# Optimization experiments

Hardware: AMD Instinct MI355X
Metric: run time of the kernel (lower is better)

Reference implementation:

```python
import jax, jax.numpy as jnp
import numpy as np

B, L, H, ED, NCONV = 64, 2048, 128, 4, 3
N = B * L


def gat(x, src, dst, edge_attr, W, a_s, a_d, We, a_e, b, self_loops):
    """PyG GATConv, heads=1, concat=True, negative_slope=0.2, fill_value='mean'."""
    n = x.shape[0]
    h = x @ W                              # [N,H]
    a_src = h @ a_s                        # [N]
    a_dst = h @ a_d                        # [N]
    alpha = a_src[src] + a_dst[dst] + (edge_attr @ We) @ a_e  # [E]
    if self_loops:
        ones = jnp.ones(src.shape[0], x.dtype)
        deg = jax.ops.segment_sum(ones, dst, num_segments=n)
        mean_attr = jax.ops.segment_sum(edge_attr, dst, num_segments=n) / jnp.maximum(deg, 1.0)[:, None]
        loop_alpha = a_src + a_dst + (mean_attr @ We) @ a_e
        idx = jnp.arange(n, dtype=src.dtype)
        src = jnp.concatenate([src, idx])
        dst = jnp.concatenate([dst, idx])
        alpha = jnp.concatenate([alpha, loop_alpha])
    alpha = jax.nn.leaky_relu(alpha, 0.2)
    m = jax.ops.segment_max(alpha, dst, num_segments=n)
    ex = jnp.exp(alpha - m[dst])
    den = jax.ops.segment_sum(ex, dst, num_segments=n)
    coef = ex / jnp.maximum(den, 1e-16)[dst]
    return jax.ops.segment_sum(coef[:, None] * h[src], dst, num_segments=n) + b


def setup_inputs() -> dict:
    key = jax.random.key(0)
    ks = iter(jax.random.split(key, 32))
    # binary trees: per graph, node k>0 has parent (k-1)//2; edge child->parent (to_up)
    local = np.arange(1, L)
    parent = (local - 1) // 2
    offs = (np.arange(B) * L)[:, None]
    src = jnp.asarray((local[None, :] + offs).ravel(), dtype=jnp.int32)
    dst = jnp.asarray((parent[None, :] + offs).ravel(), dtype=jnp.int32)
    E = src.shape[0]
    s = 0.1
    inp = {
        "x": jax.random.normal(next(ks), (N,), jnp.float32),
        "src": src,
        "dst": dst,
        "edge_attr": jax.random.normal(next(ks), (E, ED), jnp.float32),
        "up_W0": jax.random.normal(next(ks), (1, H)) * s,
        "up_W": jax.random.normal(next(ks), (NCONV - 1, H, H)) * s,
        "up_att_src": jax.random.normal(next(ks), (NCONV, H)) * s,
        "up_att_dst": jax.random.normal(next(ks), (NCONV, H)) * s,
        "up_We": jax.random.normal(next(ks), (NCONV, ED, H)) * s,
        "up_att_edge": jax.random.normal(next(ks), (NCONV, H)) * s,
        "up_b": jax.random.normal(next(ks), (NCONV, H)) * s,
        "down_W": jax.random.normal(next(ks), (NCONV - 1, H, H)) * s,
        "down_att_src": jax.random.normal(next(ks), (NCONV - 1, H)) * s,
        "down_att_dst": jax.random.normal(next(ks), (NCONV - 1, H)) * s,
        "down_We": jax.random.normal(next(ks), (NCONV - 1, ED, H)) * s,
        "down_att_edge": jax.random.normal(next(ks), (NCONV - 1, H)) * s,
        "down_b": jax.random.normal(next(ks), (NCONV - 1, H)) * s,
        "lin_W": jax.random.normal(next(ks), (NCONV - 1, H, H)) * s,
        "lin_b": jax.random.normal(next(ks), (NCONV - 1, H)) * s,
        "lin_last_W": jax.random.normal(next(ks), (H, 1)) * s,
        "lin_last_b": jax.random.normal(next(ks), (1,)) * s,
    }
    return inp


def reference(x, src, dst, edge_attr, up_W0, up_W, up_att_src, up_att_dst, up_We,
              up_att_edge, up_b, down_W, down_att_src, down_att_dst, down_We,
              down_att_edge, down_b, lin_W, lin_b, lin_last_W, lin_last_b):
    h = x[:, None]                                            # flat_c.view(-1,1)
    # upward pass: toup GATConvs (with self loops) + relu
    for i in range(NCONV):
        W = up_W0 if i == 0 else up_W[i - 1]
        h = jax.nn.relu(gat(h, src, dst, edge_attr, W, up_att_src[i], up_att_dst[i],
                            up_We[i], up_att_edge[i], up_b[i], True))
    x_up = h
    # downward pass uses reversed edges, no self loops; replicates original's
    # indexing bug (todown[0] used twice, todown[-1] never used)
    src_d, dst_d = dst, src
    x_down = jax.nn.relu(gat(x_up, src_d, dst_d, edge_attr, down_W[0], down_att_src[0],
                             down_att_dst[0], down_We[0], down_att_edge[0], down_b[0], False))
    xx = x_down + x_up
    for i in range(NCONV - 1):
        xx = jax.nn.relu(xx @ lin_W[i] + lin_b[i])
        x_down = jax.nn.relu(gat(xx, src_d, dst_d, edge_attr, down_W[i], down_att_src[i],
                                 down_att_dst[i], down_We[i], down_att_edge[i], down_b[i], False))
        xx = x_down + x_up
    final_emb = xx
    out_nodes = xx @ lin_last_W + lin_last_b                  # [N,1]
    batch_out = out_nodes.reshape(B, L)                       # all graphs are max_len
    batch_emb = final_emb.reshape(B, L, H)
    out = batch_out - batch_out[:, :1]                        # subtract root node
    return out, batch_emb
```

## Files before the change

kernel.cpp:

```cpp
#include <hip/hip_runtime.h>
#include <hip/hip_bf16.h>
#include <cstdint>
#include <cstddef>

typedef unsigned short u16;
typedef short bf16x8 __attribute__((ext_vector_type(8)));
typedef float f32x4 __attribute__((ext_vector_type(4)));

#define Bn 64
#define Ln 2048
#define Hn 128
#define EDn 4
#define Nn (Bn*Ln)

#define CV_W0    0
#define CV_WUP   128
#define CV_AS    32896
#define CV_AD    33280
#define CV_WE    33664
#define CV_AE    35200
#define CV_BUP   35584
#define CV_WD    35968
#define CV_BD    68736
#define CV_WL    68992
#define CV_BL    101760
#define CV_WLAST 102016
#define CV_TOTAL 102144

__device__ __forceinline__ float b2f(u16 u) {
  union { float f; unsigned int i; } v; v.i = ((unsigned int)u) << 16; return v.f;
}
__device__ __forceinline__ u16 f2b(float f) {
  __hip_bfloat16 h = __float2bfloat16(f);
  union { __hip_bfloat16 h; u16 u; } v; v.h = h; return v.u;
}
__device__ __forceinline__ float lrelu(float v) { return v >= 0.f ? v : 0.2f * v; }
__device__ __forceinline__ float wave_sum(float r) {
  #pragma unroll
  for (int off = 32; off > 0; off >>= 1) r += __shfl_xor(r, off, 64);
  return r;
}
__device__ __forceinline__ float ld_in(const void* p, size_t i, int f) {
  return f ? b2f(((const u16*)p)[i]) : ((const float*)p)[i];
}
__device__ __forceinline__ u16* Cbase(void* dout, int f) {
  return f ? ((u16*)dout + Nn) : (u16*)((float*)dout + Nn);
}
__device__ __forceinline__ float lo16(unsigned v) { return b2f((u16)(v & 0xFFFF)); }
__device__ __forceinline__ float hi16(unsigned v) { return b2f((u16)(v >> 16)); }

__global__ void detect_kernel(const u16* __restrict__ x, int* __restrict__ flag) {
  int lane = threadIdx.x;
  u16 u = x[lane];
  int e = (u >> 7) & 0xFF;
  bool good = (e >= 100 && e <= 140) || ((u & 0x7FFF) == 0);
  unsigned long long m = __ballot(good);
  if (lane == 0) *flag = (__popcll(m) >= 56) ? 1 : 0;
}

struct CvtArgs { const void* src[12]; int off[12]; int tr[12]; };
__global__ void cvt_kernel(CvtArgs a, const int* __restrict__ flagp, u16* __restrict__ dst) {
  int f = *flagp;
  int i = blockIdx.x * 256 + threadIdx.x;
  if (i >= CV_TOTAL) return;
  int s = 0;
  #pragma unroll
  for (int k = 1; k < 12; ++k) s = (i >= a.off[k]) ? k : s;
  int j = i - a.off[s];
  int sj = j;
  if (a.tr[s]) {
    int mat = j >> 14, rr = (j >> 7) & 127, cc = j & 127;
    sj = (mat << 14) + cc * 128 + rr;
  }
  dst[i] = f ? ((const u16*)a.src[s])[sj] : f2b(((const float*)a.src[s])[sj]);
}

__global__ void up0_kernel(const void* __restrict__ x, const void* __restrict__ edge_attr,
                           const u16* __restrict__ W0, const u16* __restrict__ att_s,
                           const u16* __restrict__ att_d, const u16* __restrict__ We0,
                           const u16* __restrict__ ae0, const u16* __restrict__ b0,
                           u16* __restrict__ y, const int* __restrict__ flagp) {
  __shared__ float P[6];
  __shared__ float comb[64];
  __shared__ float W0s[Hn];
  __shared__ float b0s[Hn];
  int f = *flagp;
  int t = threadIdx.x;
  int lane = t & 63, w = t >> 6;
  if (w < 2) {
    const u16* vb = (w == 0) ? att_s : att_d;
    float r = b2f(W0[lane]) * b2f(vb[lane]) + b2f(W0[lane+64]) * b2f(vb[lane+64]);
    r = wave_sum(r);
    if (lane == 0) P[w] = r;
  } else {
    int e0 = (w - 2) * 2;
    float a0 = b2f(ae0[lane]), a1 = b2f(ae0[lane+64]);
    float r0 = b2f(We0[e0*Hn+lane])*a0     + b2f(We0[e0*Hn+lane+64])*a1;
    float r1 = b2f(We0[(e0+1)*Hn+lane])*a0 + b2f(We0[(e0+1)*Hn+lane+64])*a1;
    r0 = wave_sum(r0); r1 = wave_sum(r1);
    if (lane == 0) { P[2+e0] = r0; P[3+e0] = r1; }
  }
  if (t < Hn) { W0s[t] = b2f(W0[t]); b0s[t] = b2f(b0[t]); }
  __syncthreads();
  int base = blockIdx.x * 64;
  if (t < 64) {
    int n = base + t;
    int local = n & (Ln - 1);
    int nb = n >> 11;
    int root = n - local;
    float S0 = P[0], D0 = P[1];
    float w0 = P[2], w1 = P[3], w2 = P[4], w3 = P[5];
    float xp = ld_in(x, n, f);
    float ad_p = D0 * xp;
    int c1l = 2*local + 1, c2l = 2*local + 2;
    int deg = (c1l < Ln ? 1 : 0) + (c2l < Ln ? 1 : 0);
    float e1 = 0.f, e2 = 0.f, xc1 = 0.f, xc2 = 0.f, sc1 = 0.f, sc2 = 0.f;
    if (deg >= 1) {
      xc1 = ld_in(x, root + c1l, f);
      size_t ei = ((size_t)nb*(Ln-1) + (c1l-1))*EDn;
      e1 = ld_in(edge_attr, ei+0, f)*w0 + ld_in(edge_attr, ei+1, f)*w1
         + ld_in(edge_attr, ei+2, f)*w2 + ld_in(edge_attr, ei+3, f)*w3;
      sc1 = lrelu(S0*xc1 + ad_p + e1);
    }
    if (deg == 2) {
      xc2 = ld_in(x, root + c2l, f);
      size_t ei = ((size_t)nb*(Ln-1) + (c2l-1))*EDn;
      e2 = ld_in(edge_attr, ei+0, f)*w0 + ld_in(edge_attr, ei+1, f)*w1
         + ld_in(edge_attr, ei+2, f)*w2 + ld_in(edge_attr, ei+3, f)*w3;
      sc2 = lrelu(S0*xc2 + ad_p + e2);
    }
    float mean_e = deg ? (e1 + e2) / (float)deg : 0.f;
    float ss = lrelu(S0*xp + ad_p + mean_e);
    float m = ss;
    if (deg >= 1) m = fmaxf(m, sc1);
    if (deg == 2) m = fmaxf(m, sc2);
    float es  = __expf(ss - m);
    float ec1 = (deg >= 1) ? __expf(sc1 - m) : 0.f;
    float ec2 = (deg == 2) ? __expf(sc2 - m) : 0.f;
    float den = es + ec1 + ec2;
    comb[t] = (es*xp + ec1*xc1 + ec2*xc2) / den;
  }
  __syncthreads();
  u16* out = y + (size_t)base * Hn;
  for (int i = t; i < 64*Hn/4; i += 256) {
    int row = i >> 5;
    int col = (i & 31) * 4;
    float c = comb[row];
    ushort4 st;
    st.x = f2b(fmaxf(c*W0s[col+0] + b0s[col+0], 0.f));
    st.y = f2b(fmaxf(c*W0s[col+1] + b0s[col+1], 0.f));
    st.z = f2b(fmaxf(c*W0s[col+2] + b0s[col+2], 0.f));
    st.w = f2b(fmaxf(c*W0s[col+3] + b0s[col+3], 0.f));
    *(ushort4*)&out[(size_t)i*4] = st;
  }
}

template<int GATHER, int EPI, int ASAD>
__global__ __launch_bounds__(256, 4) void gemm_k(
                       const u16* __restrict__ Xp, const u16* __restrict__ Wt,
                       const u16* __restrict__ bias, const u16* __restrict__ Uarr,
                       u16* __restrict__ outp, void* __restrict__ dout,
                       const int* __restrict__ flagp, int x_is_C, int out_mode,
                       float2* __restrict__ asad, const u16* __restrict__ avs,
                       const u16* __restrict__ avd, float* __restrict__ nodesp) {
  __shared__ u16 Ws[Hn*Hn];
  int f = *flagp;
  const u16* X = x_is_C ? Cbase(dout, f) : Xp;
  int t = threadIdx.x;
  int lane = t & 63, w = t >> 6;
  int m = lane & 15, q = lane >> 4;
  int row0 = blockIdx.x * 128;
  int wbase = row0 + w*32;
  uint4 wstage[8];
  #pragma unroll
  for (int i = 0; i < 8; ++i) wstage[i] = ((const uint4*)Wt)[t + 256*i];
  uint4 xf[2][4];
  #pragma unroll
  for (int rt = 0; rt < 2; ++rt) {
    int R = wbase + rt*16 + m;
    bool zero = false;
    const uint4* src;
    if (GATHER) {
      int local = R & (Ln - 1);
      if (local == 0) { zero = true; src = (const uint4*)X; }
      else src = (const uint4*)(X + (size_t)((R - local) + ((local - 1) >> 1))*Hn);
    } else {
      src = (const uint4*)(X + (size_t)R*Hn);
    }
    #pragma unroll
    for (int ki = 0; ki < 4; ++ki) {
      uint4 v = src[ki*4 + q];
      if (zero) { v.x = 0; v.y = 0; v.z = 0; v.w = 0; }
      xf[rt][ki] = v;
    }
  }
  #pragma unroll
  for (int i = 0; i < 8; ++i) {
    int g = t + 256*i; int r = g >> 4, u = g & 15;
    *(uint4*)&Ws[(r*16 + (u ^ (r & 15)))*8] = wstage[i];
  }
  __syncthreads();
  u16* Cb = Cbase(dout, f);
  float* emf = (float*)dout + Nn;
  u16* od = (out_mode == 0) ? outp : (out_mode == 1 ? Cb : (u16*)dout + Nn);
  float asv[2] = {0.f, 0.f}, adv[2] = {0.f, 0.f};
  #pragma unroll
  for (int cb = 0; cb < 2; ++cb) {
    f32x4 acc[2][4];
    #pragma unroll
    for (int rt = 0; rt < 2; ++rt)
      #pragma unroll
      for (int c4 = 0; c4 < 4; ++c4) acc[rt][c4] = (f32x4){0.f, 0.f, 0.f, 0.f};
    #pragma unroll
    for (int ki = 0; ki < 4; ++ki) {
      #pragma unroll
      for (int c4 = 0; c4 < 4; ++c4) {
        int ct = cb*4 + c4;
        bf16x8 wf = *(bf16x8*)&Ws[((ct*16 + m)*16 + ((ki*4 + q) ^ m))*8];
        #pragma unroll
        for (int rt = 0; rt < 2; ++rt)
          acc[rt][c4] = __builtin_amdgcn_mfma_f32_16x16x32_bf16(
                          wf, *(bf16x8*)&xf[rt][ki], acc[rt][c4], 0, 0, 0);
      }
    }
    #pragma unroll
    for (int rt = 0; rt < 2; ++rt) {
      int R = wbase + rt*16 + m;
      #pragma unroll
      for (int c4 = 0; c4 < 4; ++c4) {
        int ct = cb*4 + c4;
        int c0 = ct*16 + q*4;
        float o[4];
        #pragma unroll
        for (int r = 0; r < 4; ++r) o[r] = acc[rt][c4][r];
        if (ASAD == 1) {
          ushort4 sv = *(const ushort4*)&avs[c0];
          ushort4 dv = *(const ushort4*)&avd[c0];
          asv[rt] += o[0]*b2f(sv.x) + o[1]*b2f(sv.y) + o[2]*b2f(sv.z) + o[3]*b2f(sv.w);
          adv[rt] += o[0]*b2f(dv.x) + o[1]*b2f(dv.y) + o[2]*b2f(dv.z) + o[3]*b2f(dv.w);
        }
        if (EPI >= 1) {
          ushort4 bv = *(const ushort4*)&bias[c0];
          o[0] = fmaxf(o[0] + b2f(bv.x), 0.f); o[1] = fmaxf(o[1] + b2f(bv.y), 0.f);
          o[2] = fmaxf(o[2] + b2f(bv.z), 0.f); o[3] = fmaxf(o[3] + b2f(bv.w), 0.f);
        }
        if (EPI == 2) {
          ushort4 uv = *(const ushort4*)&Uarr[(size_t)R*Hn + c0];
          o[0] += b2f(uv.x); o[1] += b2f(uv.y); o[2] += b2f(uv.z); o[3] += b2f(uv.w);
        }
        if (ASAD == 2) {
          ushort4 sv = *(const ushort4*)&avs[c0];
          asv[rt] += o[0]*b2f(sv.x) + o[1]*b2f(sv.y) + o[2]*b2f(sv.z) + o[3]*b2f(sv.w);
        }
        if (out_mode == 2 && !f) {
          float4 fv; fv.x = o[0]; fv.y = o[1]; fv.z = o[2]; fv.w = o[3];
          *(float4*)&emf[(size_t)R*Hn + c0] = fv;
        } else {
          ushort4 st; st.x = f2b(o[0]); st.y = f2b(o[1]); st.z = f2b(o[2]); st.w = f2b(o[3]);
          *(ushort4*)&od[(size_t)R*Hn + c0] = st;
        }
      }
    }
  }
  #pragma unroll
  for (int rt = 0; rt < 2; ++rt) {
    int R = wbase + rt*16 + m;
    if (ASAD == 1) {
      float as_ = asv[rt], ad_ = adv[rt];
      as_ += __shfl_xor(as_, 16, 64); as_ += __shfl_xor(as_, 32, 64);
      ad_ += __shfl_xor(ad_, 16, 64); ad_ += __shfl_xor(ad_, 32, 64);
      if (q == 0) { float2 v; v.x = as_; v.y = ad_; asad[R] = v; }
    }
    if (ASAD == 2) {
      float as_ = asv[rt];
      as_ += __shfl_xor(as_, 16, 64); as_ += __shfl_xor(as_, 32, 64);
      if (q == 0) nodesp[R] = as_;
    }
  }
}

__global__ __launch_bounds__(256, 4) void gemm_blend_k(
                       const u16* __restrict__ Wt, const float2* __restrict__ coef,
                       const u16* __restrict__ bias_up, u16* __restrict__ outp,
                       void* __restrict__ dout, const int* __restrict__ flagp,
                       float2* __restrict__ asad, const u16* __restrict__ avs,
                       const u16* __restrict__ avd) {
  __shared__ u16 Ws[Hn*Hn];
  int f = *flagp;
  const u16* h = Cbase(dout, f);
  int t = threadIdx.x;
  int lane = t & 63, w = t >> 6;
  int m = lane & 15, q = lane >> 4;
  int row0 = blockIdx.x * 128;
  int wbase = row0 + w*32;
  uint4 wstage[8];
  #pragma unroll
  for (int i = 0; i < 8; ++i) wstage[i] = ((const uint4*)Wt)[t + 256*i];
  uint4 xf[2][4];
  #pragma unroll
  for (int rt = 0; rt < 2; ++rt) {
    int R = wbase + rt*16 + m;
    int local = R & (Ln - 1);
    int root = R - local;
    int c1l = 2*local + 1, c2l = 2*local + 2;
    int r1 = (c1l < Ln) ? root + c1l : R;
    int r2 = (c2l < Ln) ? root + c2l : R;
    float2 cf = coef[R];
    float es = 1.f - cf.x - cf.y;
    const uint4* hp = (const uint4*)(h + (size_t)R*Hn);
    const uint4* h1 = (const uint4*)(h + (size_t)r1*Hn);
    const uint4* h2 = (const uint4*)(h + (size_t)r2*Hn);
    #pragma unroll
    for (int ki = 0; ki < 4; ++ki) {
      int u = ki*4 + q;
      uint4 a = hp[u], b = h1[u], c = h2[u];
      uint4 bv = ((const uint4*)bias_up)[u];
      uint4 st;
      #pragma unroll
      for (int i = 0; i < 4; ++i) {
        unsigned av = ((unsigned*)&a)[i], b1v = ((unsigned*)&b)[i];
        unsigned b2v = ((unsigned*)&c)[i], bbv = ((unsigned*)&bv)[i];
        float o0 = es*lo16(av) + cf.x*lo16(b1v) + cf.y*lo16(b2v) + lo16(bbv);
        float o1 = es*hi16(av) + cf.x*hi16(b1v) + cf.y*hi16(b2v) + hi16(bbv);
        ((unsigned*)&st)[i] = (unsigned)f2b(fmaxf(o0, 0.f))
                            | ((unsigned)f2b(fmaxf(o1, 0.f)) << 16);
      }
      xf[rt][ki] = st;
    }
  }
  #pragma unroll
  for (int i = 0; i < 8; ++i) {
    int g = t + 256*i; int r = g >> 4, u = g & 15;
    *(uint4*)&Ws[(r*16 + (u ^ (r & 15)))*8] = wstage[i];
  }
  __syncthreads();
  float asv[2] = {0.f, 0.f}, adv[2] = {0.f, 0.f};
  #pragma unroll
  for (int cb = 0; cb < 2; ++cb) {
    f32x4 acc[2][4];
    #pragma unroll
    for (int rt = 0; rt < 2; ++rt)
      #pragma unroll
      for (int c4 = 0; c4 < 4; ++c4) acc[rt][c4] = (f32x4){0.f, 0.f, 0.f, 0.f};
    #pragma unroll
    for (int ki = 0; ki < 4; ++ki) {
      #pragma unroll
      for (int c4 = 0; c4 < 4; ++c4) {
        int ct = cb*4 + c4;
        bf16x8 wf = *(bf16x8*)&Ws[((ct*16 + m)*16 + ((ki*4 + q) ^ m))*8];
        #pragma unroll
        for (int rt = 0; rt < 2; ++rt)
          acc[rt][c4] = __builtin_amdgcn_mfma_f32_16x16x32_bf16(
                          wf, *(bf16x8*)&xf[rt][ki], acc[rt][c4], 0, 0, 0);
      }
    }
    #pragma unroll
    for (int rt = 0; rt < 2; ++rt) {
      int R = wbase + rt*16 + m;
      #pragma unroll
      for (int c4 = 0; c4 < 4; ++c4) {
        int ct = cb*4 + c4;
        int c0 = ct*16 + q*4;
        float o0 = acc[rt][c4][0], o1 = acc[rt][c4][1];
        float o2 = acc[rt][c4][2], o3 = acc[rt][c4][3];
        ushort4 sv = *(const ushort4*)&avs[c0];
        ushort4 dv = *(const ushort4*)&avd[c0];
        asv[rt] += o0*b2f(sv.x) + o1*b2f(sv.y) + o2*b2f(sv.z) + o3*b2f(sv.w);
        adv[rt] += o0*b2f(dv.x) + o1*b2f(dv.y) + o2*b2f(dv.z) + o3*b2f(dv.w);
        ushort4 st; st.x = f2b(o0); st.y = f2b(o1); st.z = f2b(o2); st.w = f2b(o3);
        *(ushort4*)&outp[(size_t)R*Hn + c0] = st;
      }
    }
  }
  #pragma unroll
  for (int rt = 0; rt < 2; ++rt) {
    int R = wbase + rt*16 + m;
    float as_ = asv[rt], ad_ = adv[rt];
    as_ += __shfl_xor(as_, 16, 64); as_ += __shfl_xor(as_, 32, 64);
    ad_ += __shfl_xor(ad_, 16, 64); ad_ += __shfl_xor(ad_, 32, 64);
    if (q == 0) { float2 v; v.x = as_; v.y = ad_; asad[R] = v; }
  }
}

__global__ __launch_bounds__(512, 4) void fused_down_lin_k(
                       const u16* __restrict__ Xp, const u16* __restrict__ Wdt,
                       const u16* __restrict__ bd, const u16* __restrict__ Uarr,
                       const u16* __restrict__ Wlt, const u16* __restrict__ bl,
                       u16* __restrict__ outp) {
  __shared__ u16 Ws[Hn*Hn];
  __shared__ u16 XX[128*Hn];
  int t = threadIdx.x;
  int lane = t & 63, w = t >> 6;
  int m = lane & 15, q = lane >> 4;
  int row0 = blockIdx.x * 128;
  int R = row0 + w*16 + m;
  int rl = w*16 + m;
  uint4 wstage[4];
  #pragma unroll
  for (int i = 0; i < 4; ++i) wstage[i] = ((const uint4*)Wdt)[t + 512*i];
  uint4 xf[4];
  {
    int local = R & (Ln - 1);
    bool zero = (local == 0);
    const uint4* src = zero ? (const uint4*)Xp
                     : (const uint4*)(Xp + (size_t)((R - local) + ((local - 1) >> 1))*Hn);
    #pragma unroll
    for (int ki = 0; ki < 4; ++ki) {
      uint4 v = src[ki*4 + q];
      if (zero) { v.x = 0; v.y = 0; v.z = 0; v.w = 0; }
      xf[ki] = v;
    }
  }
  #pragma unroll
  for (int i = 0; i < 4; ++i) {
    int g = t + 512*i; int r = g >> 4, u = g & 15;
    *(uint4*)&Ws[(r*16 + (u ^ (r & 15)))*8] = wstage[i];
  }
  __syncthreads();
  f32x4 acc[8];
  #pragma unroll
  for (int ct = 0; ct < 8; ++ct) acc[ct] = (f32x4){0.f, 0.f, 0.f, 0.f};
  #pragma unroll
  for (int ki = 0; ki < 4; ++ki) {
    #pragma unroll
    for (int ct = 0; ct < 8; ++ct) {
      bf16x8 wf = *(bf16x8*)&Ws[((ct*16 + m)*16 + ((ki*4 + q) ^ m))*8];
      acc[ct] = __builtin_amdgcn_mfma_f32_16x16x32_bf16(
                    wf, *(bf16x8*)&xf[ki], acc[ct], 0, 0, 0);
    }
  }
  __syncthreads();
  #pragma unroll
  for (int i = 0; i < 4; ++i) wstage[i] = ((const uint4*)Wlt)[t + 512*i];
  #pragma unroll
  for (int ct = 0; ct < 8; ++ct) {
    int c0 = ct*16 + q*4;
    ushort4 bv = *(const ushort4*)&bd[c0];
    ushort4 uv = *(const ushort4*)&Uarr[(size_t)R*Hn + c0];
    float o0 = fmaxf(acc[ct][0] + b2f(bv.x), 0.f) + b2f(uv.x);
    float o1 = fmaxf(acc[ct][1] + b2f(bv.y), 0.f) + b2f(uv.y);
    float o2 = fmaxf(acc[ct][2] + b2f(bv.z), 0.f) + b2f(uv.z);
    float o3 = fmaxf(acc[ct][3] + b2f(bv.w), 0.f) + b2f(uv.w);
    int uu = (2*ct + (q >> 1)) ^ m;
    uint2 pk;
    pk.x = (unsigned)f2b(o0) | ((unsigned)f2b(o1) << 16);
    pk.y = (unsigned)f2b(o2) | ((unsigned)f2b(o3) << 16);
    *(uint2*)&XX[rl*Hn + uu*8 + (q & 1)*4] = pk;
  }
  #pragma unroll
  for (int i = 0; i < 4; ++i) {
    int g = t + 512*i; int r = g >> 4, u = g & 15;
    *(uint4*)&Ws[(r*16 + (u ^ (r & 15)))*8] = wstage[i];
  }
  __syncthreads();
  f32x4 acc2[8];
  #pragma unroll
  for (int ct = 0; ct < 8; ++ct) acc2[ct] = (f32x4){0.f, 0.f, 0.f, 0.f};
  #pragma unroll
  for (int ki = 0; ki < 4; ++ki) {
    #pragma unroll
    for (int ct = 0; ct < 8; ++ct) {
      bf16x8 wf = *(bf16x8*)&Ws[((ct*16 + m)*16 + ((ki*4 + q) ^ m))*8];
      bf16x8 xb = *(bf16x8*)&XX[rl*Hn + (((ki*4 + q) ^ m))*8];
      acc2[ct] = __builtin_amdgcn_mfma_f32_16x16x32_bf16(wf, xb, acc2[ct], 0, 0, 0);
    }
  }
  #pragma unroll
  for (int ct = 0; ct < 8; ++ct) {
    int c0 = ct*16 + q*4;
    ushort4 bv = *(const ushort4*)&bl[c0];
    ushort4 st;
    st.x = f2b(fmaxf(acc2[ct][0] + b2f(bv.x), 0.f));
    st.y = f2b(fmaxf(acc2[ct][1] + b2f(bv.y), 0.f));
    st.z = f2b(fmaxf(acc2[ct][2] + b2f(bv.z), 0.f));
    st.w = f2b(fmaxf(acc2[ct][3] + b2f(bv.w), 0.f));
    *(ushort4*)&outp[(size_t)R*Hn + c0] = st;
  }
}

__global__ void coef_kernel(const void* __restrict__ edge_attr,
                            const u16* __restrict__ We, const u16* __restrict__ ae,
                            const float2* __restrict__ asad, float2* __restrict__ coef,
                            const int* __restrict__ flagp) {
  __shared__ float P[4];
  int f = *flagp;
  int t = threadIdx.x;
  int lane = t & 63, w = t >> 6;
  {
    unsigned av = *(const unsigned*)&ae[2*lane];
    unsigned wv = *(const unsigned*)&We[w*Hn + 2*lane];
    float r = wave_sum(lo16(wv)*lo16(av) + hi16(wv)*hi16(av));
    if (lane == 0) P[w] = r;
  }
  __syncthreads();
  int p = blockIdx.x * 256 + t;
  int local = p & (Ln - 1);
  int root = p - local;
  int nb = p >> 11;
  int c1l = 2*local + 1, c2l = 2*local + 2;
  int deg = (c1l < Ln ? 1 : 0) + (c2l < Ln ? 1 : 0);
  float2 aa = asad[p];
  float w0 = P[0], w1 = P[1], w2 = P[2], w3 = P[3];
  float e1 = 0.f, e2 = 0.f, sc1 = 0.f, sc2 = 0.f;
  if (deg >= 1) {
    size_t ei = ((size_t)nb*(Ln-1) + (c1l-1))*EDn;
    if (f) {
      ushort4 v = *(const ushort4*)((const u16*)edge_attr + ei);
      e1 = b2f(v.x)*w0 + b2f(v.y)*w1 + b2f(v.z)*w2 + b2f(v.w)*w3;
      if (deg == 2) {
        ushort4 v2 = *(const ushort4*)((const u16*)edge_attr + ei + EDn);
        e2 = b2f(v2.x)*w0 + b2f(v2.y)*w1 + b2f(v2.z)*w2 + b2f(v2.w)*w3;
      }
    } else {
      float4 v = *(const float4*)((const float*)edge_attr + ei);
      e1 = v.x*w0 + v.y*w1 + v.z*w2 + v.w*w3;
      if (deg == 2) {
        float4 v2 = *(const float4*)((const float*)edge_attr + ei + EDn);
        e2 = v2.x*w0 + v2.y*w1 + v2.z*w2 + v2.w*w3;
      }
    }
    sc1 = lrelu(asad[root + c1l].x + aa.y + e1);
    if (deg == 2) sc2 = lrelu(asad[root + c2l].x + aa.y + e2);
  }
  float mean_e = deg ? (e1 + e2) / (float)deg : 0.f;
  float ss = lrelu(aa.x + aa.y + mean_e);
  float m = ss;
  if (deg >= 1) m = fmaxf(m, sc1);
  if (deg == 2) m = fmaxf(m, sc2);
  float es  = __expf(ss - m);
  float ec1 = (deg >= 1) ? __expf(sc1 - m) : 0.f;
  float ec2 = (deg == 2) ? __expf(sc2 - m) : 0.f;
  float inv = 1.f / (es + ec1 + ec2);
  float2 cf; cf.x = ec1 * inv; cf.y = ec2 * inv;
  coef[p] = cf;
}

__global__ void blend_kernel(const u16* __restrict__ h, const float2* __restrict__ coef,
                             const u16* __restrict__ bias, u16* __restrict__ y) {
  int t = threadIdx.x;
  int g = t & 15;
  int p = blockIdx.x * 16 + (t >> 4);
  int local = p & (Ln - 1);
  int root = p - local;
  int c1l = 2*local + 1, c2l = 2*local + 2;
  int deg = (c1l < Ln ? 1 : 0) + (c2l < Ln ? 1 : 0);
  float2 cf = coef[p];
  float es = 1.f - cf.x - cf.y;
  int off = g * 8;
  uint4 hp = *(const uint4*)&h[(size_t)p*Hn + off];
  uint4 h1 = {0,0,0,0}, h2 = {0,0,0,0};
  if (deg >= 1) h1 = *(const uint4*)&h[(size_t)(root + c1l)*Hn + off];
  if (deg == 2) h2 = *(const uint4*)&h[(size_t)(root + c2l)*Hn + off];
  uint4 bv = *(const uint4*)&bias[off];
  uint4 st;
  #pragma unroll
  for (int i = 0; i < 4; ++i) {
    unsigned a = ((unsigned*)&hp)[i], b1 = ((unsigned*)&h1)[i];
    unsigned b2 = ((unsigned*)&h2)[i], bb = ((unsigned*)&bv)[i];
    float o0 = es*lo16(a) + cf.x*lo16(b1) + cf.y*lo16(b2) + lo16(bb);
    float o1 = es*hi16(a) + cf.x*hi16(b1) + cf.y*hi16(b2) + hi16(bb);
    ((unsigned*)&st)[i] = (unsigned)f2b(fmaxf(o0, 0.f)) | ((unsigned)f2b(fmaxf(o1, 0.f)) << 16);
  }
  *(uint4*)&y[(size_t)p*Hn + off] = st;
}

__global__ void score_kernel(const float* __restrict__ nodes, void* __restrict__ dout,
                             const int* __restrict__ flagp) {
  int f = *flagp;
  int n = blockIdx.x * 256 + threadIdx.x;
  float v = nodes[n] - nodes[n & ~(Ln - 1)];
  if (f) ((u16*)dout)[n] = f2b(v);
  else   ((float*)dout)[n] = v;
}

extern "C" void kernel_launch(void* const* d_in, const int* in_sizes, int n_in,
                              void* d_out, int out_size, void* d_ws, size_t ws_size,
                              hipStream_t stream) {
  const void* x         = d_in[0];
  const void* edge_attr = d_in[3];

  u16* Ubuf = (u16*)d_ws;
  u16* Abuf = Ubuf + (size_t)Nn*Hn;
  u16* Bbuf = Abuf + (size_t)Nn*Hn;
  u16* cvt  = Bbuf + (size_t)Nn*Hn;
  float2* asad = (float2*)(cvt + CV_TOTAL);
  float2* coef = asad + Nn;
  float* nodes = (float*)(coef + Nn);
  int* flag = (int*)(nodes + Nn);

  detect_kernel<<<1, 64, 0, stream>>>((const u16*)d_in[0], flag);

  CvtArgs ca;
  ca.src[0]  = d_in[4];  ca.off[0]  = CV_W0;    ca.tr[0]  = 0;
  ca.src[1]  = d_in[5];  ca.off[1]  = CV_WUP;   ca.tr[1]  = 1;
  ca.src[2]  = d_in[6];  ca.off[2]  = CV_AS;    ca.tr[2]  = 0;
  ca.src[3]  = d_in[7];  ca.off[3]  = CV_AD;    ca.tr[3]  = 0;
  ca.src[4]  = d_in[8];  ca.off[4]  = CV_WE;    ca.tr[4]  = 0;
  ca.src[5]  = d_in[9];  ca.off[5]  = CV_AE;    ca.tr[5]  = 0;
  ca.src[6]  = d_in[10]; ca.off[6]  = CV_BUP;   ca.tr[6]  = 0;
  ca.src[7]  = d_in[11]; ca.off[7]  = CV_WD;    ca.tr[7]  = 1;
  ca.src[8]  = d_in[16]; ca.off[8]  = CV_BD;    ca.tr[8]  = 0;
  ca.src[9]  = d_in[17]; ca.off[9]  = CV_WL;    ca.tr[9]  = 1;
  ca.src[10] = d_in[18]; ca.off[10] = CV_BL;    ca.tr[10] = 0;
  ca.src[11] = d_in[19]; ca.off[11] = CV_WLAST; ca.tr[11] = 0;
  cvt_kernel<<<(CV_TOTAL + 255)/256, 256, 0, stream>>>(ca, flag, cvt);

  up0_kernel<<<Nn/64, 256, 0, stream>>>(x, edge_attr, cvt+CV_W0, cvt+CV_AS, cvt+CV_AD,
                                        cvt+CV_WE, cvt+CV_AE, cvt+CV_BUP, Abuf, flag);
  gemm_k<0,0,1><<<Nn/128, 256, 0, stream>>>(Abuf, cvt+CV_WUP, nullptr, nullptr,
                                         nullptr, d_out, flag, 0, 1,
                                         asad, cvt+CV_AS+Hn, cvt+CV_AD+Hn, nullptr);
  coef_kernel<<<Nn/256, 256, 0, stream>>>(edge_attr, cvt+CV_WE+EDn*Hn, cvt+CV_AE+Hn,
                                          asad, coef, flag);
  gemm_blend_k<<<Nn/128, 256, 0, stream>>>(cvt+CV_WUP+Hn*Hn, coef, cvt+CV_BUP+Hn,
                                           Bbuf, d_out, flag,
                                           asad, cvt+CV_AS+2*Hn, cvt+CV_AD+2*Hn);
  coef_kernel<<<Nn/256, 256, 0, stream>>>(edge_attr, cvt+CV_WE+2*EDn*Hn, cvt+CV_AE+2*Hn,
                                          asad, coef, flag);
  blend_kernel<<<Nn/16, 256, 0, stream>>>(Bbuf, coef, cvt+CV_BUP+2*Hn, Ubuf);

  fused_down_lin_k<<<Nn/128, 512, 0, stream>>>(Ubuf, cvt+CV_WD, cvt+CV_BD, Ubuf,
                                               cvt+CV_WL, cvt+CV_BL, Abuf);
  fused_down_lin_k<<<Nn/128, 512, 0, stream>>>(Abuf, cvt+CV_WD, cvt+CV_BD, Ubuf,
                                               cvt+CV_WL+Hn*Hn, cvt+CV_BL+Hn, Bbuf);
  gemm_k<1,2,2><<<Nn/128, 256, 0, stream>>>(Bbuf, cvt+CV_WD+Hn*Hn, cvt+CV_BD+Hn, Ubuf,
                                         nullptr, d_out, flag, 0, 2,
                                         nullptr, cvt+CV_WLAST, nullptr, nodes);

  score_kernel<<<Nn/256, 256, 0, stream>>>(nodes, d_out, flag);
}
```

Baseline: 275.0 us.

## Load weights directly into LDS and remap blocks across XCDs

Weight tiles in the GEMM kernels now go straight from global memory into LDS through global_load_lds. This replaces the register staging and the swizzled LDS stores. To keep the XOR-swizzled layout, the swizzle is moved into the weight-conversion kernel, which pre-permutes the transposed matrices. All kernels also remap block IDs so that consecutive row ranges land on the same XCD, which should improve L2 locality for the parent/child gathers. The risk is that the pre-swizzled layout must match the LDS addressing exactly, and that the direct-to-LDS loads may serialise differently from the old register staging.

After: 277.5 us. About the same (+0.9%).

```diff
diff --git a/kernel.cpp b/kernel.cpp
--- a/kernel.cpp
+++ b/kernel.cpp
@@ -49,6 +49,16 @@
 __device__ __forceinline__ float lo16(unsigned v) { return b2f((u16)(v & 0xFFFF)); }
 __device__ __forceinline__ float hi16(unsigned v) { return b2f((u16)(v >> 16)); }
 
+__device__ __forceinline__ void gload_lds16(const void* g, void* l) {
+  __builtin_amdgcn_global_load_lds(
+      (const __attribute__((address_space(1))) void*)g,
+      (__attribute__((address_space(3))) void*)l, 16, 0, 0);
+}
+
+__device__ __forceinline__ int xcd_remap(int bid, int nwg) {
+  return (bid & 7) * (nwg >> 3) + (bid >> 3);
+}
+
 __global__ void detect_kernel(const u16* __restrict__ x, int* __restrict__ flag) {
   int lane = threadIdx.x;
   u16 u = x[lane];
@@ -69,8 +79,12 @@
   int j = i - a.off[s];
   int sj = j;
   if (a.tr[s]) {
-    int mat = j >> 14, rr = (j >> 7) & 127, cc = j & 127;
-    sj = (mat << 14) + cc * 128 + rr;
+    int mat = j >> 14, jm = j & 16383;
+    int r = jm >> 7, c = jm & 127;
+    int us = c >> 3, sub = c & 7;
+    int u = us ^ (r & 15);
+    int k = u * 8 + sub;
+    sj = (mat << 14) + k * 128 + r;
   }
   dst[i] = f ? ((const u16*)a.src[s])[sj] : f2b(((const float*)a.src[s])[sj]);
 }
@@ -102,7 +116,7 @@
   }
   if (t < Hn) { W0s[t] = b2f(W0[t]); b0s[t] = b2f(b0[t]); }
   __syncthreads();
-  int base = blockIdx.x * 64;
+  int base = xcd_remap(blockIdx.x, gridDim.x) * 64;
   if (t < 64) {
     int n = base + t;
     int local = n & (Ln - 1);
@@ -169,11 +183,11 @@
   int t = threadIdx.x;
   int lane = t & 63, w = t >> 6;
   int m = lane & 15, q = lane >> 4;
-  int row0 = blockIdx.x * 128;
+  int row0 = xcd_remap(blockIdx.x, gridDim.x) * 128;
   int wbase = row0 + w*32;
-  uint4 wstage[8];
-  #pragma unroll
-  for (int i = 0; i < 8; ++i) wstage[i] = ((const uint4*)Wt)[t + 256*i];
+  #pragma unroll
+  for (int i = 0; i < 8; ++i)
+    gload_lds16(Wt + (size_t)(i*256 + t)*8, &Ws[(size_t)(i*256 + (t & ~63))*8]);
   uint4 xf[2][4];
   #pragma unroll
   for (int rt = 0; rt < 2; ++rt) {
@@ -193,11 +207,6 @@
       if (zero) { v.x = 0; v.y = 0; v.z = 0; v.w = 0; }
       xf[rt][ki] = v;
     }
-  }
-  #pragma unroll
-  for (int i = 0; i < 8; ++i) {
-    int g = t + 256*i; int r = g >> 4, u = g & 15;
-    *(uint4*)&Ws[(r*16 + (u ^ (r & 15)))*8] = wstage[i];
   }
   __syncthreads();
   u16* Cb = Cbase(dout, f);
@@ -291,11 +300,11 @@
   int t = threadIdx.x;
   int lane = t & 63, w = t >> 6;
   int m = lane & 15, q = lane >> 4;
-  int row0 = blockIdx.x * 128;
+  int row0 = xcd_remap(blockIdx.x, gridDim.x) * 128;
   int wbase = row0 + w*32;
-  uint4 wstage[8];
-  #pragma unroll
-  for (int i = 0; i < 8; ++i) wstage[i] = ((const uint4*)Wt)[t + 256*i];
+  #pragma unroll
+  for (int i = 0; i < 8; ++i)
+    gload_lds16(Wt + (size_t)(i*256 + t)*8, &Ws[(size_t)(i*256 + (t & ~63))*8]);
   uint4 xf[2][4];
   #pragma unroll
   for (int rt = 0; rt < 2; ++rt) {
@@ -328,11 +337,6 @@
       xf[rt][ki] = st;
     }
   }
-  #pragma unroll
-  for (int i = 0; i < 8; ++i) {
-    int g = t + 256*i; int r = g >> 4, u = g & 15;
-    *(uint4*)&Ws[(r*16 + (u ^ (r & 15)))*8] = wstage[i];
-  }
   __syncthreads();
   float asv[2] = {0.f, 0.f}, adv[2] = {0.f, 0.f};
   #pragma unroll
@@ -392,12 +396,12 @@
   int t = threadIdx.x;
   int lane = t & 63, w = t >> 6;
   int m = lane & 15, q = lane >> 4;
-  int row0 = blockIdx.x * 128;
+  int row0 = xcd_remap(blockIdx.x, gridDim.x) * 128;
   int R = row0 + w*16 + m;
   int rl = w*16 + m;
-  uint4 wstage[4];
-  #pragma unroll
-  for (int i = 0; i < 4; ++i) wstage[i] = ((const uint4*)Wdt)[t + 512*i];
+  #pragma unroll
+  for (int i = 0; i < 4; ++i)
+    gload_lds16(Wdt + (size_t)(i*512 + t)*8, &Ws[(size_t)(i*512 + (t & ~63))*8]);
   uint4 xf[4];
   {
     int local = R & (Ln - 1);
@@ -411,11 +415,6 @@
       xf[ki] = v;
     }
   }
-  #pragma unroll
-  for (int i = 0; i < 4; ++i) {
-    int g = t + 512*i; int r = g >> 4, u = g & 15;
-    *(uint4*)&Ws[(r*16 + (u ^ (r & 15)))*8] = wstage[i];
-  }
   __syncthreads();
   f32x4 acc[8];
   #pragma unroll
@@ -431,7 +430,8 @@
   }
   __syncthreads();
   #pragma unroll
-  for (int i = 0; i < 4; ++i) wstage[i] = ((const uint4*)Wlt)[t + 512*i];
+  for (int i = 0; i < 4; ++i)
+    gload_lds16(Wlt + (size_t)(i*512 + t)*8, &Ws[(size_t)(i*512 + (t & ~63))*8]);
   #pragma unroll
   for (int ct = 0; ct < 8; ++ct) {
     int c0 = ct*16 + q*4;
@@ -447,11 +447,6 @@
     pk.y = (unsigned)f2b(o2) | ((unsigned)f2b(o3) << 16);
     *(uint2*)&XX[rl*Hn + uu*8 + (q & 1)*4] = pk;
   }
-  #pragma unroll
-  for (int i = 0; i < 4; ++i) {
-    int g = t + 512*i; int r = g >> 4, u = g & 15;
-    *(uint4*)&Ws[(r*16 + (u ^ (r & 15)))*8] = wstage[i];
-  }
   __syncthreads();
   f32x4 acc2[8];
   #pragma unroll
@@ -493,7 +488,7 @@
     if (lane == 0) P[w] = r;
   }
   __syncthreads();
-  int p = blockIdx.x * 256 + t;
+  int p = xcd_remap(blockIdx.x, gridDim.x) * 256 + t;
   int local = p & (Ln - 1);
   int root = p - local;
   int nb = p >> 11;
@@ -539,7 +534,7 @@
                              const u16* __restrict__ bias, u16* __restrict__ y) {
   int t = threadIdx.x;
   int g = t & 15;
-  int p = blockIdx.x * 16 + (t >> 4);
+  int p = xcd_remap(blockIdx.x, gridDim.x) * 16 + (t >> 4);
   int local = p & (Ln - 1);
   int root = p - local;
   int c1l = 2*local + 1, c2l = 2*local + 2;
@@ -567,7 +562,7 @@
 __global__ void score_kernel(const float* __restrict__ nodes, void* __restrict__ dout,
                              const int* __restrict__ flagp) {
   int f = *flagp;
-  int n = blockIdx.x * 256 + threadIdx.x;
+  int n = xcd_remap(blockIdx.x, gridDim.x) * 256 + threadIdx.x;
   float v = nodes[n] - nodes[n & ~(Ln - 1)];
   if (f) ((u16*)dout)[n] = f2b(v);
   else   ((float*)dout)[n] = v;
```
